# Optimization experiments

Measured on AMD Instinct MI355X. Metric: run time of the kernel, lower is better.

## Reference

```python
import jax, jax.numpy as jnp
import numpy as np


def setup_inputs() -> dict:
    key = jax.random.key(0)
    k1, k2, k3 = jax.random.split(key, 3)
    N, M, D = 4096, 4096, 256
    x = jax.random.normal(k1, (N, D), dtype=jnp.float32)
    y = jax.random.normal(k2, (M, D), dtype=jnp.float32)
    # torch init: normal(0.0, 0.1)
    log_band_width = 0.1 * jax.random.normal(k3, (D,), dtype=jnp.float32)
    return {"x": x, "y": y, "log_band_width": log_band_width}


def reference(x, y, log_band_width):
    # ARD kernel: k(x,y) = exp(-0.5 * sum_d (x_d - y_d)^2 / bw_d), bw = exp(log_bw)
    # Quadratic expansion to avoid the O(N*M*D) broadcast intermediate:
    # scale inputs by 1/sqrt(bw), then sqdist = |xw|^2 + |yw|^2 - 2 xw @ yw^T
    inv_sqrt_bw = jnp.exp(-0.5 * log_band_width)  # [D]
    xw = x * inv_sqrt_bw  # [N, D]
    yw = y * inv_sqrt_bw  # [M, D]
    x2 = jnp.sum(xw * xw, axis=-1)  # [N]
    y2 = jnp.sum(yw * yw, axis=-1)  # [M]
    cross = xw @ yw.T  # [N, M] GEMM
    pdist = x2[:, None] + y2[None, :] - 2.0 * cross
    pdist = jnp.maximum(pdist, 0.0)  # clamp tiny negatives from fp cancellation
    return jnp.exp(-0.5 * pdist)
```

## Files before the change

kernel.cpp:

```cpp
#include <hip/hip_runtime.h>
#include <hip/hip_bf16.h>


typedef __attribute__((ext_vector_type(8))) short bf16x8;
typedef __attribute__((ext_vector_type(4))) float f32x4;

#define NN 4096
#define MM 4096
#define DD 256

#define BM 128
#define BN 128
#define HK 128

#define GLOAD16(gp, lp)                                                        \
    __builtin_amdgcn_global_load_lds(                                          \
        (const __attribute__((address_space(1))) void*)(gp),                   \
        (__attribute__((address_space(3))) void*)(lp), 16, 0, 0)

__global__ __launch_bounds__(256) void ard_prep(
    const float* __restrict__ x, const float* __restrict__ y,
    const float* __restrict__ lbw,
    __hip_bfloat16* __restrict__ xw, __hip_bfloat16* __restrict__ yw,
    float* __restrict__ x2, float* __restrict__ y2)
{
    const int lane = threadIdx.x & 63;
    const int row  = blockIdx.x * 4 + (threadIdx.x >> 6);

    const float* src;
    __hip_bfloat16* dst;
    float* nrm;
    if (row < NN) {
        src = x + (size_t)row * DD;
        dst = xw + (size_t)row * DD;
        nrm = x2 + row;
    } else {
        const int r = row - NN;
        src = y + (size_t)r * DD;
        dst = yw + (size_t)r * DD;
        nrm = y2 + r;
    }

    const float4 v  = reinterpret_cast<const float4*>(src)[lane];
    const float4 lw = reinterpret_cast<const float4*>(lbw)[lane];

    float wv[4];
    wv[0] = v.x * __expf(-0.5f * lw.x);
    wv[1] = v.y * __expf(-0.5f * lw.y);
    wv[2] = v.z * __expf(-0.5f * lw.z);
    wv[3] = v.w * __expf(-0.5f * lw.w);

    __hip_bfloat16 h[4];
    float s = 0.0f;
#pragma unroll
    for (int j = 0; j < 4; ++j) {
        h[j] = __float2bfloat16(wv[j]);
        const float f = __bfloat162float(h[j]);
        s += f * f;
    }

    reinterpret_cast<uint2*>(dst)[lane] = *reinterpret_cast<uint2*>(h);

#pragma unroll
    for (int off = 32; off > 0; off >>= 1) s += __shfl_down(s, off);
    if (lane == 0) *nrm = s;
}

__global__ __launch_bounds__(512) void ard_gemm(
    const __hip_bfloat16* __restrict__ A,
    const __hip_bfloat16* __restrict__ B,
    const float* __restrict__ x2, const float* __restrict__ y2,
    float* __restrict__ out)
{
    __shared__ __align__(16) __hip_bfloat16 sA[2][BM * HK];
    __shared__ __align__(16) __hip_bfloat16 sB[2][BN * HK];

    const int tid  = threadIdx.x;
    const int lane = tid & 63;
    const int wid  = tid >> 6;
    const int wr   = wid >> 2;
    const int wc   = wid & 3;

    const int bi = blockIdx.y;
    const int bj = blockIdx.x;
    const size_t arow0 = (size_t)bi * BM;
    const size_t brow0 = (size_t)bj * BN;

    const int crow = lane >> 4;
    const int slot = lane & 15;

    auto stage = [&](int h) {
        const int colb = h * 256;
#pragma unroll
        for (int t = 0; t < 4; ++t) {
            const int r   = wid * 16 + t * 4;
            const int row = r + crow;
            const int lcb = colb + ((slot * 16) ^ ((row & 7) << 4));
            GLOAD16((const char*)(A + (arow0 + row) * DD) + lcb,
                    (char*)&sA[h][0] + r * 256);
            GLOAD16((const char*)(B + (brow0 + row) * DD) + lcb,
                    (char*)&sB[h][0] + r * 256);
        }
    };

    f32x4 acc[4][2] = {};
    const int frow = lane & 15;
    const int fkb  = (lane >> 4) * 16;
    const int swz  = (frow & 7) << 4;

    stage(0);
    __syncthreads();
    stage(1);

#pragma unroll
    for (int h = 0; h < 2; ++h) {
        if (h == 1) __syncthreads();
#pragma unroll
        for (int kk = 0; kk < 4; ++kk) {
            const int kb = kk * 64 + fkb;
            bf16x8 a[4], b[2];
#pragma unroll
            for (int m = 0; m < 4; ++m) {
                const int row = wr * 64 + m * 16 + frow;
                a[m] = *reinterpret_cast<const bf16x8*>(
                    (const char*)&sA[h][0] + row * 256 + (kb ^ swz));
            }
#pragma unroll
            for (int n = 0; n < 2; ++n) {
                const int row = wc * 32 + n * 16 + frow;
                b[n] = *reinterpret_cast<const bf16x8*>(
                    (const char*)&sB[h][0] + row * 256 + (kb ^ swz));
            }
#pragma unroll
            for (int m = 0; m < 4; ++m)
#pragma unroll
                for (int n = 0; n < 2; ++n)
                    acc[m][n] = __builtin_amdgcn_mfma_f32_16x16x32_bf16(
                        b[n], a[m], acc[m][n], 0, 0, 0);
        }
    }

    const int row0 = bi * BM + wr * 64;
    const int col0 = bj * BN + wc * 32;
    const int cl   = lane & 15;
    const int rsub = (lane >> 4) * 4;

#pragma unroll
    for (int m = 0; m < 4; ++m) {
        const int r = row0 + m * 16 + cl;
        const float xv = x2[r];
        float* orow = out + (size_t)r * MM;
#pragma unroll
        for (int n = 0; n < 2; ++n) {
            const int c = col0 + n * 16 + rsub;
            const float4 yv = *reinterpret_cast<const float4*>(y2 + c);
            f32x4 o;
            o.x = __expf(-0.5f * fmaxf(xv + yv.x - 2.0f * acc[m][n][0], 0.0f));
            o.y = __expf(-0.5f * fmaxf(xv + yv.y - 2.0f * acc[m][n][1], 0.0f));
            o.z = __expf(-0.5f * fmaxf(xv + yv.z - 2.0f * acc[m][n][2], 0.0f));
            o.w = __expf(-0.5f * fmaxf(xv + yv.w - 2.0f * acc[m][n][3], 0.0f));
            __builtin_nontemporal_store(o, reinterpret_cast<f32x4*>(orow + c));
        }
    }
}

extern "C" void kernel_launch(void* const* d_in, const int* in_sizes, int n_in,
                              void* d_out, int out_size, void* d_ws, size_t ws_size,
                              hipStream_t stream) {
    const float* x   = (const float*)d_in[0];
    const float* y   = (const float*)d_in[1];
    const float* lbw = (const float*)d_in[2];
    float* out = (float*)d_out;

    char* ws = (char*)d_ws;
    __hip_bfloat16* xw = (__hip_bfloat16*)ws;
    __hip_bfloat16* yw = (__hip_bfloat16*)(ws + (size_t)2 * 1024 * 1024);
    float* x2 = (float*)(ws + (size_t)4 * 1024 * 1024);
    float* y2 = (float*)(ws + (size_t)4 * 1024 * 1024 + 16384);

    ard_prep<<<(NN + MM) / 4, 256, 0, stream>>>(x, y, lbw, xw, yw, x2, y2);

    dim3 grid(MM / BN, NN / BM);
    ard_gemm<<<grid, 512, 0, stream>>>(xw, yw, x2, y2, out);
}
```

Baseline: 35.83 us.

## Use 4 waves with larger per-wave tiles and stage epilogue through LDS

Cuts the GEMM block from 8 to 4 waves, so each wave now computes a 64x64 tile (4x4 MFMA accumulators) and reuses each loaded A/B fragment across more MFMAs. The epilogue writes results into a padded LDS buffer that reuses the operand shared memory, then stores full contiguous 512-byte rows to global memory with nontemporal stores. The aim is more coalesced output writes for the 64 MB result and less LDS read traffic per MFMA. In exchange there are more registers per thread, fewer waves to hide latency, and two extra barriers plus an LDS round trip.

```diff
diff --git a/kernel.cpp b/kernel.cpp
--- a/kernel.cpp
+++ b/kernel.cpp
@@ -12,6 +12,7 @@
 #define BM 128
 #define BN 128
 #define HK 128
+#define EPLD 132
 
 #define GLOAD16(gp, lp)                                                        \
     __builtin_amdgcn_global_load_lds(                                          \
@@ -66,20 +67,22 @@
     if (lane == 0) *nrm = s;
 }
 
-__global__ __launch_bounds__(512) void ard_gemm(
+__global__ __launch_bounds__(256) void ard_gemm(
     const __hip_bfloat16* __restrict__ A,
     const __hip_bfloat16* __restrict__ B,
     const float* __restrict__ x2, const float* __restrict__ y2,
     float* __restrict__ out)
 {
-    __shared__ __align__(16) __hip_bfloat16 sA[2][BM * HK];
-    __shared__ __align__(16) __hip_bfloat16 sB[2][BN * HK];
+    __shared__ __align__(16) char smem[131072];
+    char* sAh[2] = { smem,         smem + 32768 };
+    char* sBh[2] = { smem + 65536, smem + 98304 };
+    float* ep = reinterpret_cast<float*>(smem);
 
     const int tid  = threadIdx.x;
     const int lane = tid & 63;
     const int wid  = tid >> 6;
-    const int wr   = wid >> 2;
-    const int wc   = wid & 3;
+    const int wr   = wid >> 1;
+    const int wc   = wid & 1;
 
     const int bi = blockIdx.y;
     const int bj = blockIdx.x;
@@ -92,18 +95,16 @@
     auto stage = [&](int h) {
         const int colb = h * 256;
 #pragma unroll
-        for (int t = 0; t < 4; ++t) {
-            const int r   = wid * 16 + t * 4;
+        for (int t = 0; t < 8; ++t) {
+            const int r   = wid * 32 + t * 4;
             const int row = r + crow;
             const int lcb = colb + ((slot * 16) ^ ((row & 7) << 4));
-            GLOAD16((const char*)(A + (arow0 + row) * DD) + lcb,
-                    (char*)&sA[h][0] + r * 256);
-            GLOAD16((const char*)(B + (brow0 + row) * DD) + lcb,
-                    (char*)&sB[h][0] + r * 256);
+            GLOAD16((const char*)(A + (arow0 + row) * DD) + lcb, sAh[h] + r * 256);
+            GLOAD16((const char*)(B + (brow0 + row) * DD) + lcb, sBh[h] + r * 256);
         }
     };
 
-    f32x4 acc[4][2] = {};
+    f32x4 acc[4][4] = {};
     const int frow = lane & 15;
     const int fkb  = (lane >> 4) * 16;
     const int swz  = (frow & 7) << 4;
@@ -118,49 +119,60 @@
 #pragma unroll
         for (int kk = 0; kk < 4; ++kk) {
             const int kb = kk * 64 + fkb;
-            bf16x8 a[4], b[2];
+            bf16x8 a[4], b[4];
 #pragma unroll
             for (int m = 0; m < 4; ++m) {
                 const int row = wr * 64 + m * 16 + frow;
-                a[m] = *reinterpret_cast<const bf16x8*>(
-                    (const char*)&sA[h][0] + row * 256 + (kb ^ swz));
+                a[m] = *reinterpret_cast<const bf16x8*>(sAh[h] + row * 256 + (kb ^ swz));
             }
 #pragma unroll
-            for (int n = 0; n < 2; ++n) {
-                const int row = wc * 32 + n * 16 + frow;
-                b[n] = *reinterpret_cast<const bf16x8*>(
-                    (const char*)&sB[h][0] + row * 256 + (kb ^ swz));
+            for (int n = 0; n < 4; ++n) {
+                const int row = wc * 64 + n * 16 + frow;
+                b[n] = *reinterpret_cast<const bf16x8*>(sBh[h] + row * 256 + (kb ^ swz));
             }
 #pragma unroll
             for (int m = 0; m < 4; ++m)
 #pragma unroll
-                for (int n = 0; n < 2; ++n)
+                for (int n = 0; n < 4; ++n)
                     acc[m][n] = __builtin_amdgcn_mfma_f32_16x16x32_bf16(
                         b[n], a[m], acc[m][n], 0, 0, 0);
         }
     }
 
-    const int row0 = bi * BM + wr * 64;
-    const int col0 = bj * BN + wc * 32;
+    __syncthreads();
+
     const int cl   = lane & 15;
     const int rsub = (lane >> 4) * 4;
+    const int row0 = bi * BM;
+    const int col0 = bj * BN;
 
 #pragma unroll
     for (int m = 0; m < 4; ++m) {
-        const int r = row0 + m * 16 + cl;
-        const float xv = x2[r];
-        float* orow = out + (size_t)r * MM;
+        const int rl = wr * 64 + m * 16 + cl;
+        const float xv = x2[row0 + rl];
 #pragma unroll
-        for (int n = 0; n < 2; ++n) {
-            const int c = col0 + n * 16 + rsub;
-            const float4 yv = *reinterpret_cast<const float4*>(y2 + c);
+        for (int n = 0; n < 4; ++n) {
+            const int c = wc * 64 + n * 16 + rsub;
+            const float4 yv = *reinterpret_cast<const float4*>(y2 + col0 + c);
             f32x4 o;
             o.x = __expf(-0.5f * fmaxf(xv + yv.x - 2.0f * acc[m][n][0], 0.0f));
             o.y = __expf(-0.5f * fmaxf(xv + yv.y - 2.0f * acc[m][n][1], 0.0f));
             o.z = __expf(-0.5f * fmaxf(xv + yv.z - 2.0f * acc[m][n][2], 0.0f));
             o.w = __expf(-0.5f * fmaxf(xv + yv.w - 2.0f * acc[m][n][3], 0.0f));
-            __builtin_nontemporal_store(o, reinterpret_cast<f32x4*>(orow + c));
+            *reinterpret_cast<f32x4*>(&ep[rl * EPLD + c]) = o;
         }
+    }
+
+    __syncthreads();
+
+    const int srow2 = tid >> 5;
+    const int cfl   = (tid & 31) * 4;
+#pragma unroll
+    for (int i = 0; i < 16; ++i) {
+        const int row = i * 8 + srow2;
+        const f32x4 v = *reinterpret_cast<const f32x4*>(&ep[row * EPLD + cfl]);
+        __builtin_nontemporal_store(
+            v, reinterpret_cast<f32x4*>(out + (size_t)(row0 + row) * MM + col0 + cfl));
     }
 }
 
@@ -181,5 +193,5 @@
     ard_prep<<<(NN + MM) / 4, 256, 0, stream>>>(x, y, lbw, xw, yw, x2, y2);
 
     dim3 grid(MM / BN, NN / BM);
-    ard_gemm<<<grid, 512, 0, stream>>>(xw, yw, x2, y2, out);
+    ard_gemm<<<grid, 256, 0, stream>>>(xw, yw, x2, y2, out);
 }
```

Result: slower. 38.01 us (+6.1%).
